# Performance work log

Hardware: AMD Instinct MI355X
Metric: run time of the kernel (lower is better)

Reference implementation:

```python
import jax, jax.numpy as jnp
import numpy as np

N_NODES = 50000
N_EDGES = 800000
NFEAT, NHID, NCLASS = 512, 128, 40


def setup_inputs() -> dict:
    key = jax.random.key(0)
    ks = jax.random.split(key, 8)
    stdv1 = 1.0 / np.sqrt(NHID)
    stdv2 = 1.0 / np.sqrt(NCLASS)
    x = jax.random.normal(ks[0], (N_NODES, NFEAT), dtype=jnp.float32)
    W1 = jax.random.uniform(ks[1], (NFEAT, NHID), jnp.float32, -stdv1, stdv1)
    b1 = jax.random.uniform(ks[2], (NHID,), jnp.float32, -stdv1, stdv1)
    W2 = jax.random.uniform(ks[3], (NHID, NCLASS), jnp.float32, -stdv2, stdv2)
    b2 = jax.random.uniform(ks[4], (NCLASS,), jnp.float32, -stdv2, stdv2)
    edge_src = jax.random.randint(ks[5], (N_EDGES,), 0, N_NODES, dtype=jnp.int32)
    edge_dst = jax.random.randint(ks[6], (N_EDGES,), 0, N_NODES, dtype=jnp.int32)
    # normalized adjacency weights (positive, ~1/deg scale)
    edge_w = jax.random.uniform(ks[7], (N_EDGES,), jnp.float32, 0.0, 2.0 / 16.0)
    return {"x": x, "W1": W1, "b1": b1, "W2": W2, "b2": b2,
            "edge_src": edge_src, "edge_dst": edge_dst, "edge_w": edge_w}


def _spmm(edge_src, edge_dst, edge_w, support, n_nodes):
    # out[i] = sum_{e: dst(e)=i} w_e * support[src(e)]  == spmm(adj, support)
    msgs = edge_w[:, None] * support[edge_src]          # [E, F]
    return jax.ops.segment_sum(msgs, edge_dst, num_segments=n_nodes)


def reference(x, W1, b1, W2, b2, edge_src, edge_dst, edge_w):
    # layer 1: dense transform then sparse aggregation, bias, relu
    support = x @ W1                                     # [N, nhid]
    h = _spmm(edge_src, edge_dst, edge_w, support, x.shape[0]) + b1
    h = jax.nn.relu(h)
    # dropout is identity in eval mode
    # layer 2
    support2 = h @ W2                                    # [N, nclass]
    out = _spmm(edge_src, edge_dst, edge_w, support2, x.shape[0]) + b2
    return out
```

## Files before the change

### kernel.cpp

```cpp
#include <hip/hip_runtime.h>
#include <hip/hip_bf16.h>


#define NFEAT 512
#define NHID  128
#define NCLS  40
#define BSH   8
#define SLOTSH 6
#define BSLOT 6144
#define ACHUNK 2048

typedef __attribute__((ext_vector_type(8))) short bf16x8;
typedef __attribute__((ext_vector_type(4))) float f32x4;
typedef __fp16 cvt16x2 __attribute__((ext_vector_type(2)));
typedef _Float16 h16x2 __attribute__((ext_vector_type(2)));

__device__ inline short f2bf(float f) {
  __hip_bfloat16 b = __float2bfloat16(f);
  return *reinterpret_cast<short*>(&b);
}

__device__ inline bf16x8 cvt8(float4 a, float4 b) {
  bf16x8 r;
  r[0] = f2bf(a.x); r[1] = f2bf(a.y); r[2] = f2bf(a.z); r[3] = f2bf(a.w);
  r[4] = f2bf(b.x); r[5] = f2bf(b.y); r[6] = f2bf(b.z); r[7] = f2bf(b.w);
  return r;
}

__device__ inline unsigned pk2u(cvt16x2 v) { union { cvt16x2 h; unsigned u; } x; x.h = v; return x.u; }
__device__ inline h16x2   u2a(unsigned u)  { union { h16x2 h; unsigned u; } x; x.u = u; return x.h; }

__global__ __launch_bounds__(256) void w1t_zero(
    const float* __restrict__ W1, __hip_bfloat16* __restrict__ W1t,
    int4* __restrict__ zp, int n4) {
  __shared__ float t[64][129];
  const int tid = threadIdx.x;
  if (blockIdx.x < 8) {
    const int k0 = blockIdx.x * 64;
#pragma unroll
    for (int i = 0; i < 8; ++i) {
      int f = i * 256 + tid;
      int r = f >> 5, c = (f & 31) << 2;
      float4 v = *(const float4*)&W1[(size_t)(k0 + r) * NHID + c];
      t[r][c] = v.x; t[r][c + 1] = v.y; t[r][c + 2] = v.z; t[r][c + 3] = v.w;
    }
    __syncthreads();
#pragma unroll
    for (int i = 0; i < 32; ++i) {
      int o = i * 256 + tid;
      int k = o & 63, n = o >> 6;
      W1t[(size_t)n * NFEAT + k0 + k] = __float2bfloat16(t[k][n]);
    }
  } else {
    int i = (blockIdx.x - 8) * 256 + tid;
    if (i < n4) zp[i] = make_int4(0, 0, 0, 0);
  }
}

__device__ __forceinline__ void gemm1_body(
    char* smem, const float* __restrict__ x, const __hip_bfloat16* __restrict__ W1t,
    _Float16* __restrict__ support, int nrows, int bid) {
  char* sA0 = smem;
  char* sB0 = smem + 16384;
  const int tid = threadIdx.x;
  const int lane = tid & 63;
  const int wid = tid >> 6;
  const int wm = wid >> 1, wn = wid & 1;
  const int row0 = bid * 64;
  const int l15 = lane & 15, l4 = lane >> 4;

  const int s_ar = tid >> 2;
  const int s_ac = (tid & 3) * 16;
  const int s_br = tid >> 1;
  const int s_bc = (tid & 1) * 32;
  const bool a_ok = (row0 + s_ar) < nrows;
  const float* aptr = &x[(size_t)(row0 + s_ar) * NFEAT + s_ac];
  const uint4* bptr = (const uint4*)&W1t[(size_t)s_br * NFEAT + s_bc];

  f32x4 acc[2][4];
#pragma unroll
  for (int m = 0; m < 2; ++m)
#pragma unroll
    for (int n = 0; n < 4; ++n) acc[m][n] = (f32x4){0.f, 0.f, 0.f, 0.f};

  float4 ra0[4], ra1[4];
  uint4 rb0[4], rb1[4];

  auto LOADAB = [&](int kt, int sel) {
    if (sel == 0) {
      if (a_ok) {
        const float4* p = (const float4*)(aptr + (size_t)kt * 64);
#pragma unroll
        for (int i = 0; i < 4; ++i) ra0[i] = p[i];
      } else {
        float4 z = make_float4(0.f, 0.f, 0.f, 0.f);
#pragma unroll
        for (int i = 0; i < 4; ++i) ra0[i] = z;
      }
      const uint4* q = bptr + (size_t)kt * 8;
#pragma unroll
      for (int i = 0; i < 4; ++i) rb0[i] = q[i];
    } else {
      if (a_ok) {
        const float4* p = (const float4*)(aptr + (size_t)kt * 64);
#pragma unroll
        for (int i = 0; i < 4; ++i) ra1[i] = p[i];
      } else {
        float4 z = make_float4(0.f, 0.f, 0.f, 0.f);
#pragma unroll
        for (int i = 0; i < 4; ++i) ra1[i] = z;
      }
      const uint4* q = bptr + (size_t)kt * 8;
#pragma unroll
      for (int i = 0; i < 4; ++i) rb1[i] = q[i];
    }
  };
  auto WRITE = [&](int buf, int sel) {
    bf16x8 c0, c1;
    if (sel == 0) { c0 = cvt8(ra0[0], ra0[1]); c1 = cvt8(ra0[2], ra0[3]); }
    else          { c0 = cvt8(ra1[0], ra1[1]); c1 = cvt8(ra1[2], ra1[3]); }
    int swa = (s_ar & 7) << 4;
    char* sA = sA0 + buf * 8192;
    *(bf16x8*)(sA + ((s_ar * 128 + s_ac * 2) ^ swa)) = c0;
    *(bf16x8*)(sA + ((s_ar * 128 + s_ac * 2 + 16) ^ swa)) = c1;
    int swb = (s_br & 7) << 4;
    char* sB = sB0 + buf * 16384;
#pragma unroll
    for (int i = 0; i < 4; ++i) {
      uint4 v = (sel == 0) ? rb0[i] : rb1[i];
      *(uint4*)(sB + ((s_br * 128 + s_bc * 2 + i * 16) ^ swb)) = v;
    }
  };
  auto COMP = [&](int buf) {
    char* sA = sA0 + buf * 8192;
    char* sB = sB0 + buf * 16384;
#pragma unroll
    for (int kk = 0; kk < 64; kk += 32) {
      bf16x8 a[2], b[4];
      int cb = (kk + l4 * 8) * 2;
#pragma unroll
      for (int m = 0; m < 2; ++m) {
        int r = wm * 32 + m * 16 + l15;
        a[m] = *(const bf16x8*)(sA + ((r * 128 + cb) ^ ((r & 7) << 4)));
      }
#pragma unroll
      for (int n = 0; n < 4; ++n) {
        int r = wn * 64 + n * 16 + l15;
        b[n] = *(const bf16x8*)(sB + ((r * 128 + cb) ^ ((r & 7) << 4)));
      }
#pragma unroll
      for (int m = 0; m < 2; ++m)
#pragma unroll
        for (int n = 0; n < 4; ++n)
          acc[m][n] = __builtin_amdgcn_mfma_f32_16x16x32_bf16(a[m], b[n], acc[m][n], 0, 0, 0);
    }
  };
  auto BAR = [&]() {
    asm volatile("s_waitcnt lgkmcnt(0)" ::: "memory");
    __builtin_amdgcn_sched_barrier(0);
    __builtin_amdgcn_s_barrier();
    __builtin_amdgcn_sched_barrier(0);
  };

  LOADAB(0, 0);
  LOADAB(1, 1);
  WRITE(0, 0);
  LOADAB(2, 0);
  BAR();

#pragma unroll
  for (int t = 0; t < 8; ++t) {
    if (t < 7) {
      if ((t + 1) & 1) {
        WRITE(1, 1);
        if (t + 3 < 8) LOADAB(t + 3, 1);
      } else {
        WRITE(0, 0);
        if (t + 3 < 8) LOADAB(t + 3, 0);
      }
    }
    COMP(t & 1);
    if (t < 7) BAR();
  }

#pragma unroll
  for (int m = 0; m < 2; ++m) {
#pragma unroll
    for (int r = 0; r < 4; ++r) {
      int grow = row0 + wm * 32 + m * 16 + l4 * 4 + r;
      if (grow < nrows) {
#pragma unroll
        for (int n = 0; n < 4; ++n) {
          int col = wn * 64 + n * 16 + l15;
          support[(size_t)grow * NHID + col] = (_Float16)acc[m][n][r];
        }
      }
    }
  }
}

__device__ __forceinline__ void bucketize_body(
    char* smem, const int* __restrict__ esrc, const int* __restrict__ edst,
    const float* __restrict__ ew, int* __restrict__ bcur, int* __restrict__ deg,
    int* __restrict__ bsrc, float* __restrict__ bw, int* __restrict__ bdst,
    int E, int nb, int bid) {
  int* lh = (int*)smem;
  int* lo = lh + 256;
  int* gbase = lo + 256;
  int* s_src = gbase + 256;
  float* s_w = (float*)(s_src + ACHUNK);
  int* s_dst = (int*)(s_w + ACHUNK);
  const int tid = threadIdx.x;
  const int base = bid * ACHUNK;
  const int cnt = min(ACHUNK, E - base);

  for (int t = tid; t < nb; t += 256) lh[t] = 0;
  __syncthreads();

  int my_s[8], my_d[8], my_t[8];
  float my_w[8];
#pragma unroll
  for (int i = 0; i < 8; ++i) {
    int idx = base + i * 256 + tid;
    if (idx < E) {
      my_s[i] = esrc[idx];
      my_d[i] = edst[idx];
      my_w[i] = ew[idx];
      my_t[i] = atomicAdd(&lh[my_d[i] >> BSH], 1);
      atomicAdd(&deg[my_d[i]], 1);
    }
  }
  __syncthreads();
  if (tid == 0) {
    int run = 0;
    for (int b = 0; b < nb; ++b) { lo[b] = run; run += lh[b]; }
  }
  __syncthreads();
  if (tid < nb && lh[tid] > 0)
    gbase[tid] = tid * BSLOT + atomicAdd(&bcur[tid], lh[tid]);
  __syncthreads();
#pragma unroll
  for (int i = 0; i < 8; ++i) {
    int idx = base + i * 256 + tid;
    if (idx < E) {
      int p = lo[my_d[i] >> BSH] + my_t[i];
      s_src[p] = my_s[i];
      s_w[p] = my_w[i];
      s_dst[p] = my_d[i];
    }
  }
  __syncthreads();
  for (int j = tid; j < cnt; j += 256) {
    int d = s_dst[j];
    int b = d >> BSH;
    int g = gbase[b] + (j - lo[b]);
    bsrc[g] = s_src[j];
    bw[g] = s_w[j];
    bdst[g] = d;
  }
}

__global__ __launch_bounds__(256, 3) void fat_kernel(
    const float* __restrict__ x, const __hip_bfloat16* __restrict__ W1t,
    _Float16* __restrict__ support, int nrows,
    const int* __restrict__ esrc, const int* __restrict__ edst,
    const float* __restrict__ ew, int* __restrict__ bcur, int* __restrict__ deg,
    int* __restrict__ bsrc, float* __restrict__ bw, int* __restrict__ bdst,
    int E, int nb) {
  __shared__ __align__(16) char smem[49152];
  const int bid = (int)blockIdx.x;
  if (bid % 3 == 2)
    bucketize_body(smem, esrc, edst, ew, bcur, deg, bsrc, bw, bdst, E, nb, bid / 3);
  else
    gemm1_body(smem, x, W1t, support, nrows, bid - bid / 3);
}

__global__ __launch_bounds__(256) void bucket_scatter(
    const int* __restrict__ bcur, const int* __restrict__ bsrc,
    const float* __restrict__ bw, const int* __restrict__ bdst,
    int2* __restrict__ cwsrc, int n) {
  __shared__ int cur[1 << BSH];
  const int tid = threadIdx.x;
  const int d0 = blockIdx.x << BSH;
  for (int t = tid; t < (1 << BSH); t += 256) cur[t] = (d0 + t) << SLOTSH;
  __syncthreads();
  const int bstart = blockIdx.x * BSLOT;
  const int bend = bstart + bcur[blockIdx.x];
  for (int j = bstart + tid; j < bend; j += 256) {
    int d = bdst[j];
    int slot = atomicAdd(&cur[d - d0], 1);
    float w = bw[j];
    cwsrc[slot] = make_int2(bsrc[j], (int)pk2u(__builtin_amdgcn_cvt_pkrtz(w, w)));
  }
}

__global__ __launch_bounds__(1024) void spmm1_fused(
    const int* __restrict__ deg, const int2* __restrict__ cwsrc,
    const _Float16* __restrict__ support, const float* __restrict__ b1,
    const float* __restrict__ W2, _Float16* __restrict__ s2, int n) {
  __shared__ __align__(16) char sW[48 * 128 * 2];
  __shared__ __align__(16) char sH[16 * 128 * 2];
  const int tid = threadIdx.x;
  for (int i = tid; i < 48 * 128; i += 1024) {
    int nn = i >> 7, k = i & 127;
    float v = (nn < NCLS) ? W2[k * NCLS + nn] : 0.f;
    int byte = (nn * 256 + k * 2) ^ ((nn & 7) << 4);
    *(short*)(sW + byte) = f2bf(v);
  }

  const int wv = tid >> 6, f2 = tid & 63;
  const int node0 = blockIdx.x * 16;
  const int node = node0 + wv;
  const float2 bb = *(const float2*)&b1[f2 * 2];
  const unsigned* sp = (const unsigned*)support;

  const int dg = (node < n) ? deg[node] : 0;
  int2 eself = (f2 < dg) ? cwsrc[((size_t)node << SLOTSH) + f2] : make_int2(0, 0);
  h16x2 accA = (h16x2){(_Float16)0, (_Float16)0};
  h16x2 accB = (h16x2){(_Float16)0, (_Float16)0};
  int j = 0;
  for (; j + 7 < dg; j += 8) {
#pragma unroll
    for (int q = 0; q < 8; ++q) {
      int s = __builtin_amdgcn_readlane(eself.x, j + q);
      unsigned w2u = (unsigned)__builtin_amdgcn_readlane(eself.y, j + q);
      unsigned u = sp[((size_t)(unsigned)s << 6) | (unsigned)f2];
      if (q & 1) accB += u2a(u) * u2a(w2u);
      else       accA += u2a(u) * u2a(w2u);
    }
  }
  for (; j < dg; ++j) {
    int s = __builtin_amdgcn_readlane(eself.x, j);
    unsigned w2u = (unsigned)__builtin_amdgcn_readlane(eself.y, j);
    unsigned u = sp[((size_t)(unsigned)s << 6) | (unsigned)f2];
    if (j & 1) accB += u2a(u) * u2a(w2u);
    else       accA += u2a(u) * u2a(w2u);
  }
  h16x2 acc2 = accA + accB;
  float a0 = fmaxf((float)acc2[0] + bb.x, 0.f);
  float a1 = fmaxf((float)acc2[1] + bb.y, 0.f);
  {
    int byte = (wv * 256 + f2 * 4) ^ ((wv & 7) << 4);
    unsigned pair = (unsigned)(unsigned short)f2bf(a0) |
                    ((unsigned)(unsigned short)f2bf(a1) << 16);
    *(unsigned*)(sH + byte) = pair;
  }
  __syncthreads();
  if (wv < 3) {
    const int l15 = f2 & 15, l4 = f2 >> 4;
    f32x4 acc = (f32x4){0.f, 0.f, 0.f, 0.f};
#pragma unroll
    for (int kk = 0; kk < 4; ++kk) {
      int ka = (kk * 32 + l4 * 8) * 2;
      bf16x8 af = *(const bf16x8*)(sH + ((l15 * 256 + ka) ^ ((l15 & 7) << 4)));
      int nrow = wv * 16 + l15;
      bf16x8 bf = *(const bf16x8*)(sW + ((nrow * 256 + ka) ^ ((nrow & 7) << 4)));
      acc = __builtin_amdgcn_mfma_f32_16x16x32_bf16(af, bf, acc, 0, 0, 0);
    }
    int col = wv * 16 + l15;
    if (col < NCLS) {
#pragma unroll
      for (int r = 0; r < 4; ++r) {
        int onode = node0 + l4 * 4 + r;
        if (onode < n) s2[(size_t)onode * NCLS + col] = (_Float16)acc[r];
      }
    }
  }
}

__global__ __launch_bounds__(256) void spmm2_gather(
    const int* __restrict__ deg, const int2* __restrict__ cwsrc,
    const _Float16* __restrict__ s2,
    const float* __restrict__ b2, float* __restrict__ out, int n) {
  const int w = threadIdx.x >> 6;
  const int f2 = threadIdx.x & 63;
  const int node = blockIdx.x * 4 + w;
  if (node >= n) return;
  const int dg = deg[node];
  int2 eself = (f2 < dg) ? cwsrc[((size_t)node << SLOTSH) + f2] : make_int2(0, 0);
  const unsigned f2c = (f2 < 20) ? (unsigned)f2 : 0u;
  h16x2 accA = (h16x2){(_Float16)0, (_Float16)0};
  h16x2 accB = (h16x2){(_Float16)0, (_Float16)0};
  const unsigned* sp = (const unsigned*)s2;
  int j = 0;
  for (; j + 7 < dg; j += 8) {
#pragma unroll
    for (int q = 0; q < 8; ++q) {
      int s = __builtin_amdgcn_readlane(eself.x, j + q);
      unsigned w2u = (unsigned)__builtin_amdgcn_readlane(eself.y, j + q);
      unsigned u = sp[(size_t)(unsigned)s * 20u + f2c];
      if (q & 1) accB += u2a(u) * u2a(w2u);
      else       accA += u2a(u) * u2a(w2u);
    }
  }
  for (; j < dg; ++j) {
    int s = __builtin_amdgcn_readlane(eself.x, j);
    unsigned w2u = (unsigned)__builtin_amdgcn_readlane(eself.y, j);
    unsigned u = sp[(size_t)(unsigned)s * 20u + f2c];
    if (j & 1) accB += u2a(u) * u2a(w2u);
    else       accA += u2a(u) * u2a(w2u);
  }
  if (f2 < 20) {
    h16x2 acc2 = accA + accB;
    float2 o;
    o.x = (float)acc2[0] + b2[f2 * 2];
    o.y = (float)acc2[1] + b2[f2 * 2 + 1];
    *(float2*)&out[(size_t)node * NCLS + f2 * 2] = o;
  }
}

extern "C" void kernel_launch(void* const* d_in, const int* in_sizes, int n_in,
                              void* d_out, int out_size, void* d_ws, size_t ws_size,
                              hipStream_t stream) {
  const float* x   = (const float*)d_in[0];
  const float* W1  = (const float*)d_in[1];
  const float* b1  = (const float*)d_in[2];
  const float* W2  = (const float*)d_in[3];
  const float* b2  = (const float*)d_in[4];
  const int* esrc  = (const int*)d_in[5];
  const int* edst  = (const int*)d_in[6];
  const float* ew  = (const float*)d_in[7];
  float* out = (float*)d_out;

  const int N = in_sizes[0] / NFEAT;
  const int E = in_sizes[5];
  const int NB = (N + (1 << BSH) - 1) >> BSH;

  char* ws = (char*)d_ws;
  size_t off = 0;
  auto alloc = [&](size_t bytes) {
    void* p = ws + off;
    off += (bytes + 255) & ~(size_t)255;
    return p;
  };
  int2*  cwsrc = (int2*)alloc((size_t)N * (1 << SLOTSH) * 8);
  int*   degb  = (int*)alloc((size_t)((N + NB + 3) & ~3) * 4);
  int*   deg   = degb;
  int*   bcur  = degb + N;
  int*   bsrc  = (int*)alloc((size_t)NB * BSLOT * 4);
  float* bw    = (float*)alloc((size_t)NB * BSLOT * 4);
  int*   bdst  = (int*)alloc((size_t)NB * BSLOT * 4);
  __hip_bfloat16* W1t = (__hip_bfloat16*)alloc((size_t)NHID * NFEAT * 2);
  _Float16* support   = (_Float16*)alloc((size_t)N * NHID * 2);
  _Float16* s2        = (_Float16*)alloc((size_t)N * NCLS * 2);

  const int nz4 = (N + NB + 3) / 4;
  w1t_zero<<<8 + (nz4 + 255) / 256, 256, 0, stream>>>(W1, W1t, (int4*)degb, nz4);

  const int GEMMB = (N + 63) / 64;
  const int BUCKB = (E + ACHUNK - 1) / ACHUNK;
  fat_kernel<<<GEMMB + BUCKB, 256, 0, stream>>>(
      x, W1t, support, N,
      esrc, edst, ew, bcur, deg, bsrc, bw, bdst, E, NB);

  bucket_scatter<<<NB, 256, 0, stream>>>(bcur, bsrc, bw, bdst, cwsrc, N);

  spmm1_fused<<<(N + 15) / 16, 1024, 0, stream>>>(deg, cwsrc, support, b1, W2, s2, N);

  spmm2_gather<<<(N + 3) / 4, 256, 0, stream>>>(deg, cwsrc, s2, b2, out, N);
}
```

Before: 157.5 us.

## Split fused SpMM1+GEMM2 into feature-sliced gather kernel and separate MFMA GEMM

The fused 1024-thread kernel, where each wave walked all edges of one node serially over 128 features, is split in two. The first new kernel gives each block one 32-feature slice of 4 nodes. Each wave processes 4 edges at once using 16-lane groups and reduces them with cross-lane shuffles, then writes bf16 hidden activations to a scratch buffer that reuses bsrc. The second kernel loads those activations into LDS and runs the MFMA projection by W2. The goal is more memory-level parallelism in the edge gather, at the cost of an extra hidden-activation round trip through global memory and one more launch.

```diff
diff --git a/kernel.cpp b/kernel.cpp
--- a/kernel.cpp
+++ b/kernel.cpp
@@ -294,58 +294,74 @@
   }
 }
 
-__global__ __launch_bounds__(1024) void spmm1_fused(
+__global__ __launch_bounds__(256) void spmm1_slice(
     const int* __restrict__ deg, const int2* __restrict__ cwsrc,
-    const _Float16* __restrict__ support, const float* __restrict__ b1,
-    const float* __restrict__ W2, _Float16* __restrict__ s2, int n) {
+    const unsigned* __restrict__ supu, const float* __restrict__ b1,
+    unsigned* __restrict__ hu, int n) {
+  const int tid = threadIdx.x;
+  const int wv = tid >> 6, lane = tid & 63;
+  const int g = lane >> 4, fi = lane & 15;
+  const int bid = (int)blockIdx.x;
+  const int slice = bid & 3;
+  const int node = (bid >> 2) * 4 + wv;
+  if (node >= n) return;
+  const int dg = deg[node];
+  int2 eself = (lane < dg) ? cwsrc[((size_t)node << SLOTSH) + lane] : make_int2(0, 0);
+  const unsigned boff = (unsigned)(slice * 16 + fi);
+  h16x2 accA = (h16x2){(_Float16)0, (_Float16)0};
+  h16x2 accB = (h16x2){(_Float16)0, (_Float16)0};
+  const int iters = (dg + 3) >> 2;
+  for (int kk = 0; kk < iters; kk += 2) {
+    int j0 = g + kk * 4;
+    int j1 = j0 + 4;
+    int j0c = (j0 < dg) ? j0 : 0;
+    int j1c = (j1 < dg) ? j1 : 0;
+    int s0 = __shfl(eself.x, j0c, 64);
+    unsigned w0 = (unsigned)__shfl(eself.y, j0c, 64);
+    int s1 = __shfl(eself.x, j1c, 64);
+    unsigned w1 = (unsigned)__shfl(eself.y, j1c, 64);
+    if (j0 >= dg) w0 = 0u;
+    if (j1 >= dg || kk + 1 >= iters) w1 = 0u;
+    unsigned u0 = supu[((size_t)(unsigned)s0 << 6) | boff];
+    unsigned u1 = supu[((size_t)(unsigned)s1 << 6) | boff];
+    accA += u2a(u0) * u2a(w0);
+    accB += u2a(u1) * u2a(w1);
+  }
+  h16x2 acc = accA + accB;
+  acc += u2a((unsigned)__shfl_xor(*(int*)&acc, 16, 64));
+  acc += u2a((unsigned)__shfl_xor(*(int*)&acc, 32, 64));
+  if (lane < 16) {
+    const float2 bb = *(const float2*)&b1[slice * 32 + fi * 2];
+    float a0 = fmaxf((float)acc[0] + bb.x, 0.f);
+    float a1 = fmaxf((float)acc[1] + bb.y, 0.f);
+    unsigned pair = (unsigned)(unsigned short)f2bf(a0) |
+                    ((unsigned)(unsigned short)f2bf(a1) << 16);
+    hu[((size_t)node << 6) | boff] = pair;
+  }
+}
+
+__global__ __launch_bounds__(256) void gemm2_mfma(
+    const unsigned* __restrict__ hu, const float* __restrict__ W2,
+    _Float16* __restrict__ s2, int n) {
   __shared__ __align__(16) char sW[48 * 128 * 2];
   __shared__ __align__(16) char sH[16 * 128 * 2];
   const int tid = threadIdx.x;
-  for (int i = tid; i < 48 * 128; i += 1024) {
+  for (int i = tid; i < 48 * 128; i += 256) {
     int nn = i >> 7, k = i & 127;
     float v = (nn < NCLS) ? W2[k * NCLS + nn] : 0.f;
     int byte = (nn * 256 + k * 2) ^ ((nn & 7) << 4);
     *(short*)(sW + byte) = f2bf(v);
   }
-
+  const int node0 = blockIdx.x * 16;
+  for (int i = tid; i < 16 * 64; i += 256) {
+    int r = i >> 6, k2 = i & 63;
+    int nd = node0 + r;
+    unsigned v = (nd < n) ? hu[((size_t)nd << 6) | (unsigned)k2] : 0u;
+    int byte = (r * 256 + k2 * 4) ^ ((r & 7) << 4);
+    *(unsigned*)(sH + byte) = v;
+  }
+  __syncthreads();
   const int wv = tid >> 6, f2 = tid & 63;
-  const int node0 = blockIdx.x * 16;
-  const int node = node0 + wv;
-  const float2 bb = *(const float2*)&b1[f2 * 2];
-  const unsigned* sp = (const unsigned*)support;
-
-  const int dg = (node < n) ? deg[node] : 0;
-  int2 eself = (f2 < dg) ? cwsrc[((size_t)node << SLOTSH) + f2] : make_int2(0, 0);
-  h16x2 accA = (h16x2){(_Float16)0, (_Float16)0};
-  h16x2 accB = (h16x2){(_Float16)0, (_Float16)0};
-  int j = 0;
-  for (; j + 7 < dg; j += 8) {
-#pragma unroll
-    for (int q = 0; q < 8; ++q) {
-      int s = __builtin_amdgcn_readlane(eself.x, j + q);
-      unsigned w2u = (unsigned)__builtin_amdgcn_readlane(eself.y, j + q);
-      unsigned u = sp[((size_t)(unsigned)s << 6) | (unsigned)f2];
-      if (q & 1) accB += u2a(u) * u2a(w2u);
-      else       accA += u2a(u) * u2a(w2u);
-    }
-  }
-  for (; j < dg; ++j) {
-    int s = __builtin_amdgcn_readlane(eself.x, j);
-    unsigned w2u = (unsigned)__builtin_amdgcn_readlane(eself.y, j);
-    unsigned u = sp[((size_t)(unsigned)s << 6) | (unsigned)f2];
-    if (j & 1) accB += u2a(u) * u2a(w2u);
-    else       accA += u2a(u) * u2a(w2u);
-  }
-  h16x2 acc2 = accA + accB;
-  float a0 = fmaxf((float)acc2[0] + bb.x, 0.f);
-  float a1 = fmaxf((float)acc2[1] + bb.y, 0.f);
-  {
-    int byte = (wv * 256 + f2 * 4) ^ ((wv & 7) << 4);
-    unsigned pair = (unsigned)(unsigned short)f2bf(a0) |
-                    ((unsigned)(unsigned short)f2bf(a1) << 16);
-    *(unsigned*)(sH + byte) = pair;
-  }
-  __syncthreads();
   if (wv < 3) {
     const int l15 = f2 & 15, l4 = f2 >> 4;
     f32x4 acc = (f32x4){0.f, 0.f, 0.f, 0.f};
@@ -443,6 +459,7 @@
   __hip_bfloat16* W1t = (__hip_bfloat16*)alloc((size_t)NHID * NFEAT * 2);
   _Float16* support   = (_Float16*)alloc((size_t)N * NHID * 2);
   _Float16* s2        = (_Float16*)alloc((size_t)N * NCLS * 2);
+  unsigned* hu = (unsigned*)bsrc;
 
   const int nz4 = (N + NB + 3) / 4;
   w1t_zero<<<8 + (nz4 + 255) / 256, 256, 0, stream>>>(W1, W1t, (int4*)degb, nz4);
@@ -455,7 +472,11 @@
 
   bucket_scatter<<<NB, 256, 0, stream>>>(bcur, bsrc, bw, bdst, cwsrc, N);
 
-  spmm1_fused<<<(N + 15) / 16, 1024, 0, stream>>>(deg, cwsrc, support, b1, W2, s2, N);
+  const int NGRP = (N + 3) / 4;
+  spmm1_slice<<<NGRP * 4, 256, 0, stream>>>(
+      deg, cwsrc, (const unsigned*)support, b1, hu, N);
+
+  gemm2_mfma<<<(N + 15) / 16, 256, 0, stream>>>(hu, W2, s2, N);
 
   spmm2_gather<<<(N + 3) / 4, 256, 0, stream>>>(deg, cwsrc, s2, b2, out, N);
 }
```

Result: slower. 197.8 us (+25.5%).
